# Kernel tuning notes

Hardware: AMD Instinct MI355X
Metric: run time of the kernel (lower is better)

The kernel has to match this reference:

```python
import jax, jax.numpy as jnp
import numpy as np

B, N, D = 2, 2048, 1024
H, DH = 16, 64
DI = 4096
EPS = 1e-5
NEG_SLOPE = 0.01  # F.leaky_relu default


def _ln(x, g, b):
    mu = jnp.mean(x, axis=-1, keepdims=True)
    var = jnp.mean((x - mu) ** 2, axis=-1, keepdims=True)
    return (x - mu) * jax.lax.rsqrt(var + EPS) * g + b


def setup_inputs() -> dict:
    key = jax.random.key(0)
    ks = jax.random.split(key, 10)
    s = 0.02
    return {
        "Z": jax.random.normal(ks[0], (B, N, D), jnp.float32),
        "new_mask": jax.random.normal(ks[1], (B, N, N), jnp.float32),
        "mask": jax.random.uniform(ks[2], (B, N, N), jnp.float32),
        "ln1_g": jnp.ones((D,), jnp.float32),
        "ln1_b": jnp.zeros((D,), jnp.float32),
        "qkv_w": jax.random.normal(ks[3], (3 * D, D), jnp.float32) * s,
        "qkv_b": jnp.zeros((3 * D,), jnp.float32),
        "o_w": jax.random.normal(ks[4], (D, H * DH), jnp.float32) * s,
        "ln2_g": jnp.ones((D,), jnp.float32),
        "ln2_b": jnp.zeros((D,), jnp.float32),
        "p1_w": jax.random.normal(ks[5], (DI, D), jnp.float32) * s,
        "p1_b": jnp.zeros((DI,), jnp.float32),
        "p2_w": jax.random.normal(ks[6], (D, DI), jnp.float32) * s,
        "p2_b": jnp.zeros((D,), jnp.float32),
    }


def reference(Z, new_mask, mask, ln1_g, ln1_b, qkv_w, qkv_b, o_w, ln2_g, ln2_b, p1_w, p1_b, p2_w, p2_b):
    inp = Z
    Zn = _ln(Z, ln1_g, ln1_b)
    qkv = (Zn @ qkv_w.T + qkv_b).reshape(B, N, H, 3 * DH)
    # torch chunk order in the source: V, Q, K
    V, Q, K = jnp.split(qkv, 3, axis=3)  # each [B,N,H,DH]
    # scores: einsum('bnij,bmij->binm') == [B,H,N,N]
    W = jnp.einsum("bnhd,bmhd->bhnm", Q, K) / np.sqrt(DH) + new_mask[:, None]
    A = jax.nn.softmax(W, axis=3) * mask[:, None]
    attn = jnp.einsum("bhnm,bmhd->bnhd", A, V).reshape(B, N, D)
    attn = jnp.where(attn >= 0, attn, NEG_SLOPE * attn) @ o_w.T  # leaky_relu then o_net (no bias)
    Z1 = attn + inp
    Zn2 = _ln(Z1, ln2_g, ln2_b)
    h = jax.nn.relu(Zn2 @ p1_w.T + p1_b)
    return h @ p2_w.T + p2_b + Z1
```

## Files before the change

kernel.cpp:

```cpp
#include <hip/hip_runtime.h>

typedef unsigned short u16;
typedef __attribute__((ext_vector_type(8))) short bf16x8;
typedef __attribute__((ext_vector_type(4))) float f32x4;

#define DEV static __device__ __forceinline__

DEV u16 f2bf(float f) {
    unsigned u = __float_as_uint(f);
    u += 0x7FFFu + ((u >> 16) & 1u);
    return (u16)(u >> 16);
}

typedef const __attribute__((address_space(1))) void* gas1_t;
typedef __attribute__((address_space(3))) void* gas3_t;

DEV void gl_lds16(const u16* g, u16* l) {
    __builtin_amdgcn_global_load_lds((gas1_t)g, (gas3_t)l, 16, 0, 0);
}

DEV int sw8(int row, int chunk) { return row * 64 + ((chunk ^ (row & 7)) << 3); }

__global__ void cast_bf16(const float* __restrict__ in, u16* __restrict__ out, int n4) {
    int i = blockIdx.x * blockDim.x + threadIdx.x;
    if (i < n4) {
        float4 v = ((const float4*)in)[i];
        ushort4 o;
        o.x = f2bf(v.x); o.y = f2bf(v.y); o.z = f2bf(v.z); o.w = f2bf(v.w);
        ((ushort4*)out)[i] = o;
    }
}

__global__ void cast_qkv(const float* __restrict__ in, u16* __restrict__ out) {
    int i = blockIdx.x * 256 + threadIdx.x;
    int orow = i >> 8, cc = i & 255;
    int region = orow >> 10, rem = orow & 1023, h = rem >> 6, t = rem & 63;
    int srow = h * 192 + region * 64 + t;
    float4 v = ((const float4*)in)[srow * 256 + cc];
    ushort4 o;
    o.x = f2bf(v.x); o.y = f2bf(v.y); o.z = f2bf(v.z); o.w = f2bf(v.w);
    ((ushort4*)out)[i] = o;
}

__global__ void permute_bias(const float* __restrict__ in, float* __restrict__ out) {
    int i = blockIdx.x * 256 + threadIdx.x;
    if (i < 3072) {
        int region = i >> 10, rem = i & 1023, h = rem >> 6, t = rem & 63;
        out[i] = in[h * 192 + region * 64 + t];
    }
}

__global__ void pack_mask(const float* __restrict__ nm, const float* __restrict__ pm,
                          unsigned* __restrict__ out, int n4) {
    int i = blockIdx.x * blockDim.x + threadIdx.x;
    if (i < n4) {
        float4 a = ((const float4*)nm)[i];
        float4 b = ((const float4*)pm)[i];
        uint4 o;
        o.x = ((unsigned)f2bf(b.x) << 16) | f2bf(a.x * 1.4426950f);
        o.y = ((unsigned)f2bf(b.y) << 16) | f2bf(a.y * 1.4426950f);
        o.z = ((unsigned)f2bf(b.z) << 16) | f2bf(a.z * 1.4426950f);
        o.w = ((unsigned)f2bf(b.w) << 16) | f2bf(a.w * 1.4426950f);
        ((uint4*)out)[i] = o;
    }
}

__global__ __launch_bounds__(256) void ln_bf16(const float* __restrict__ x,
                                               const float* __restrict__ gam,
                                               const float* __restrict__ bet,
                                               u16* __restrict__ y) {
    const int row = blockIdx.x;
    const int t = threadIdx.x;
    const float4 v = ((const float4*)(x + (size_t)row * 1024))[t];
    float s = v.x + v.y + v.z + v.w;
    float ss = v.x * v.x + v.y * v.y + v.z * v.z + v.w * v.w;
#pragma unroll
    for (int o = 1; o < 64; o <<= 1) {
        s += __shfl_xor(s, o);
        ss += __shfl_xor(ss, o);
    }
    __shared__ float rs[4], rss[4];
    const int wave = t >> 6, lane = t & 63;
    if (lane == 0) { rs[wave] = s; rss[wave] = ss; }
    __syncthreads();
    const float tot = rs[0] + rs[1] + rs[2] + rs[3];
    const float totss = rss[0] + rss[1] + rss[2] + rss[3];
    const float mu = tot * (1.0f / 1024.0f);
    const float var = totss * (1.0f / 1024.0f) - mu * mu;
    const float rstd = rsqrtf(var + 1e-5f);
    const float4 g4 = ((const float4*)gam)[t];
    const float4 b4 = ((const float4*)bet)[t];
    ushort4 o;
    o.x = f2bf((v.x - mu) * rstd * g4.x + b4.x);
    o.y = f2bf((v.y - mu) * rstd * g4.y + b4.y);
    o.z = f2bf((v.z - mu) * rstd * g4.z + b4.z);
    o.w = f2bf((v.w - mu) * rstd * g4.w + b4.w);
    ((ushort4*)(y + (size_t)row * 1024))[t] = o;
}

__global__ __launch_bounds__(256) void ln2_comb(const float* __restrict__ p0,
                                                const float* __restrict__ p1,
                                                const float* __restrict__ Z,
                                                const float* __restrict__ gam,
                                                const float* __restrict__ bet,
                                                float* __restrict__ Z1,
                                                u16* __restrict__ y) {
    const int row = blockIdx.x;
    const int t = threadIdx.x;
    const float4 a = ((const float4*)(p0 + (size_t)row * 1024))[t];
    const float4 c = ((const float4*)(p1 + (size_t)row * 1024))[t];
    const float4 z = ((const float4*)(Z + (size_t)row * 1024))[t];
    float4 v;
    v.x = a.x + c.x + z.x; v.y = a.y + c.y + z.y;
    v.z = a.z + c.z + z.z; v.w = a.w + c.w + z.w;
    ((float4*)(Z1 + (size_t)row * 1024))[t] = v;
    float s = v.x + v.y + v.z + v.w;
    float ss = v.x * v.x + v.y * v.y + v.z * v.z + v.w * v.w;
#pragma unroll
    for (int o = 1; o < 64; o <<= 1) {
        s += __shfl_xor(s, o);
        ss += __shfl_xor(ss, o);
    }
    __shared__ float rs[4], rss[4];
    const int wave = t >> 6, lane = t & 63;
    if (lane == 0) { rs[wave] = s; rss[wave] = ss; }
    __syncthreads();
    const float tot = rs[0] + rs[1] + rs[2] + rs[3];
    const float totss = rss[0] + rss[1] + rss[2] + rss[3];
    const float mu = tot * (1.0f / 1024.0f);
    const float var = totss * (1.0f / 1024.0f) - mu * mu;
    const float rstd = rsqrtf(var + 1e-5f);
    const float4 g4 = ((const float4*)gam)[t];
    const float4 b4 = ((const float4*)bet)[t];
    ushort4 o;
    o.x = f2bf((v.x - mu) * rstd * g4.x + b4.x);
    o.y = f2bf((v.y - mu) * rstd * g4.y + b4.y);
    o.z = f2bf((v.z - mu) * rstd * g4.z + b4.z);
    o.w = f2bf((v.w - mu) * rstd * g4.w + b4.w);
    ((ushort4*)(y + (size_t)row * 1024))[t] = o;
}

__global__ __launch_bounds__(256) void out_comb(const float* __restrict__ p0,
                                                const float* __restrict__ p1,
                                                const float* __restrict__ bias,
                                                const float* __restrict__ Z1,
                                                float* __restrict__ out) {
    int i = blockIdx.x * 256 + threadIdx.x;
    float4 a = ((const float4*)p0)[i];
    float4 c = ((const float4*)p1)[i];
    float4 z = ((const float4*)Z1)[i];
    float4 b = ((const float4*)bias)[i & 255];
    float4 o;
    o.x = a.x + c.x + z.x + b.x; o.y = a.y + c.y + z.y + b.y;
    o.z = a.z + c.z + z.z + b.z; o.w = a.w + c.w + z.w + b.w;
    ((float4*)out)[i] = o;
}

template <int EPI>
__global__ __launch_bounds__(256, 2) void gemm_bt(const u16* __restrict__ A,
                                                  const u16* __restrict__ Bt,
                                                  const float* __restrict__ bias,
                                                  void* __restrict__ out0,
                                                  void* __restrict__ out1,
                                                  void* __restrict__ out2,
                                                  int M, int N, int K, int ldk) {
    __shared__ __align__(16) u16 As[128 * 32];
    __shared__ __align__(16) u16 Bs[128 * 32];
    const int tid = threadIdx.x;
    const int wave = tid >> 6, lane = tid & 63;
    const int lhi = lane >> 4, llo = lane & 15;
    const int bx = blockIdx.x, by = blockIdx.y;
    const int kz = blockIdx.z * K;

    const int arow = wave * 32 + (lane >> 2);
    const int acol = (lane & 3) * 8;
    const u16* gA = A + (size_t)(by * 128 + arow) * ldk + kz + acol;
    const u16* gB = Bt + (size_t)(bx * 128 + arow) * ldk + kz + acol;
    u16* lA = As + wave * 1024 + lane * 8;
    u16* lB = Bs + wave * 1024 + lane * 8;

    const int wr = wave >> 1, wc = wave & 1;
    const f32x4 zero = {0.f, 0.f, 0.f, 0.f};
    f32x4 acc[4][4];
#pragma unroll
    for (int i = 0; i < 4; i++)
#pragma unroll
        for (int j = 0; j < 4; j++) acc[i][j] = zero;

    for (int k0 = 0; k0 < K; k0 += 32) {
        __syncthreads();
        gl_lds16(gA, lA);
        gl_lds16(gA + 16 * (size_t)ldk, lA + 512);
        gl_lds16(gB, lB);
        gl_lds16(gB + 16 * (size_t)ldk, lB + 512);
        gA += 32; gB += 32;
        __syncthreads();
        bf16x8 af[4], bfr[4];
#pragma unroll
        for (int i = 0; i < 4; i++)
            af[i] = *(const bf16x8*)(As + (wr * 64 + i * 16 + llo) * 32 + lhi * 8);
#pragma unroll
        for (int j = 0; j < 4; j++)
            bfr[j] = *(const bf16x8*)(Bs + (wc * 64 + j * 16 + llo) * 32 + lhi * 8);
#pragma unroll
        for (int i = 0; i < 4; i++)
#pragma unroll
            for (int j = 0; j < 4; j++)
                acc[i][j] = __builtin_amdgcn_mfma_f32_16x16x32_bf16(af[i], bfr[j], acc[i][j], 0, 0, 0);
    }

    const int rbase = by * 128 + wr * 64 + lhi * 4;
    const int cbase = bx * 128 + wc * 64 + llo;
    float* pout = (EPI == 4) ? ((float*)out0 + (size_t)blockIdx.z * M * N) : (float*)out0;
#pragma unroll
    for (int i = 0; i < 4; i++) {
#pragma unroll
        for (int j = 0; j < 4; j++) {
#pragma unroll
            for (int r = 0; r < 4; r++) {
                const int row = rbase + i * 16 + r;
                const int col = cbase + j * 16;
                float v = acc[i][j][r];
                if constexpr (EPI == 0) {
                    v += bias[col];
                    const int region = col >> 10;
                    const int c = col & 1023;
                    const int b = row >> 11, n = row & 2047;
                    if (region == 0) {
                        ((float*)out0)[(size_t)row * 1024 + c] = v;
                    } else {
                        const int h = c >> 6, t = c & 63;
                        u16* dst = (region == 1) ? (u16*)out1 : (u16*)out2;
                        dst[(((size_t)(b * 16 + h)) * 2048 + n) * 64 + t] = f2bf(v);
                    }
                } else if constexpr (EPI == 2) {
                    v += bias[col];
                    v = v > 0.f ? v : 0.f;
                    ((u16*)out0)[(size_t)row * N + col] = f2bf(v);
                } else {
                    pout[(size_t)row * N + col] = v;
                }
            }
        }
    }
}

__global__ __launch_bounds__(256) void vtrans(const float* __restrict__ Vsc,
                                              u16* __restrict__ Vt) {
    __shared__ u16 Ts[64 * 72];
    const int nt = blockIdx.x;
    const int bh = blockIdx.y;
    const int b = bh >> 4, h = bh & 15;
    const int t = threadIdx.x;
    const int n0 = nt * 64;
    const int nr = t >> 2;
    const int dq = (t & 3) * 16;
    const float* src = Vsc + ((size_t)(b * 2048 + n0 + nr)) * 1024 + h * 64 + dq;
    float4 v0 = ((const float4*)src)[0];
    float4 v1 = ((const float4*)src)[1];
    float4 v2 = ((const float4*)src)[2];
    float4 v3 = ((const float4*)src)[3];
    u16* c0 = Ts + nr;
    c0[(dq + 0) * 72]  = f2bf(v0.x); c0[(dq + 1) * 72]  = f2bf(v0.y);
    c0[(dq + 2) * 72]  = f2bf(v0.z); c0[(dq + 3) * 72]  = f2bf(v0.w);
    c0[(dq + 4) * 72]  = f2bf(v1.x); c0[(dq + 5) * 72]  = f2bf(v1.y);
    c0[(dq + 6) * 72]  = f2bf(v1.z); c0[(dq + 7) * 72]  = f2bf(v1.w);
    c0[(dq + 8) * 72]  = f2bf(v2.x); c0[(dq + 9) * 72]  = f2bf(v2.y);
    c0[(dq + 10) * 72] = f2bf(v2.z); c0[(dq + 11) * 72] = f2bf(v2.w);
    c0[(dq + 12) * 72] = f2bf(v3.x); c0[(dq + 13) * 72] = f2bf(v3.y);
    c0[(dq + 14) * 72] = f2bf(v3.z); c0[(dq + 15) * 72] = f2bf(v3.w);
    __syncthreads();
    const int d = t >> 2, n8 = (t & 3) * 16;
    bf16x8 o0 = *(const bf16x8*)(Ts + d * 72 + n8);
    bf16x8 o1 = *(const bf16x8*)(Ts + d * 72 + n8 + 8);
    u16* dst = Vt + ((size_t)bh * 64 + d) * 2048 + n0 + n8;
    *(bf16x8*)dst = o0;
    *(bf16x8*)(dst + 8) = o1;
}

__global__ __launch_bounds__(256, 4) void attn_fused4(const u16* __restrict__ Qg,
                                                      const u16* __restrict__ Kg,
                                                      const u16* __restrict__ Vt,
                                                      const unsigned* __restrict__ Mp,
                                                      u16* __restrict__ attnL) {
    __shared__ __align__(16) u16 Qs[64 * 64];
    __shared__ __align__(16) u16 Ks[64 * 64];
    __shared__ __align__(16) u16 Vs[64 * 64];
    __shared__ __align__(16) u16 Ps[64 * 72];
    const int tid = threadIdx.x, wave = tid >> 6, lane = tid & 63;
    const int lhi = lane >> 4, llo = lane & 15;
    const int id = blockIdx.x;
    const int hh = id >> 6, rem = id & 63;
    const int b = rem >> 5, qt = rem & 31;
    const int bh = b * 16 + hh;
    const int q0 = qt * 64;
    const int l3 = lane >> 3, l7 = lane & 7;
    const int swcol = (l7 ^ (l3 & 7)) * 8;

#pragma unroll
    for (int s = 0; s < 2; s++) {
        const int row = wave * 16 + s * 8 + l3;
        gl_lds16(Qg + ((size_t)bh * 2048 + q0 + row) * 64 + swcol,
                 Qs + wave * 1024 + s * 512 + lane * 8);
    }

    const unsigned* Mpb = Mp + (size_t)b * 2048 * 2048;
    int midx[4];
#pragma unroll
    for (int r = 0; r < 4; r++)
        midx[r] = (q0 + wave * 16 + lhi * 4 + r) * 2048 + llo;

    const f32x4 zero = {0.f, 0.f, 0.f, 0.f};
    f32x4 accO[4];
    float lsum[4];
#pragma unroll
    for (int j = 0; j < 4; j++) accO[j] = zero;
#pragma unroll
    for (int r = 0; r < 4; r++) lsum[r] = 0.f;

    const float CS = 0.125f * 1.4426950f;
    const int pb0 = (wave * 16 + lhi * 4) * 72 + llo;

    for (int m0 = 0; m0 < 2048; m0 += 64) {
        __syncthreads();
#pragma unroll
        for (int s = 0; s < 2; s++) {
            const int row = wave * 16 + s * 8 + l3;
            gl_lds16(Kg + ((size_t)bh * 2048 + m0 + row) * 64 + swcol,
                     Ks + wave * 1024 + s * 512 + lane * 8);
            gl_lds16(Vt + ((size_t)bh * 64 + row) * 2048 + m0 + swcol,
                     Vs + wave * 1024 + s * 512 + lane * 8);
        }
        unsigned mv[4][4];
#pragma unroll
        for (int r = 0; r < 4; r++)
#pragma unroll
            for (int j = 0; j < 4; j++) mv[r][j] = Mpb[midx[r] + m0 + j * 16];
        __syncthreads();

        f32x4 sacc[4];
#pragma unroll
        for (int j = 0; j < 4; j++) sacc[j] = zero;
#pragma unroll
        for (int kk = 0; kk < 2; kk++) {
            const bf16x8 aq = *(const bf16x8*)(Qs + sw8(wave * 16 + llo, kk * 4 + lhi));
#pragma unroll
            for (int j = 0; j < 4; j++) {
                const bf16x8 bk = *(const bf16x8*)(Ks + sw8(j * 16 + llo, kk * 4 + lhi));
                sacc[j] = __builtin_amdgcn_mfma_f32_16x16x32_bf16(aq, bk, sacc[j], 0, 0, 0);
            }
        }

#pragma unroll
        for (int j = 0; j < 4; j++)
#pragma unroll
            for (int r = 0; r < 4; r++) {
                const unsigned u = mv[r][j];
                const float nm = __uint_as_float(u << 16);
                const float pm = __uint_as_float(u & 0xFFFF0000u);
                const float e = exp2f(fmaf(sacc[j][r], CS, nm));
                lsum[r] += e;
                const float p = e * pm;
                Ps[pb0 + r * 72 + j * 16] = (u16)((__float_as_uint(p) + 0x8000u) >> 16);
            }

#pragma unroll
        for (int kk = 0; kk < 2; kk++) {
            const bf16x8 ap = *(const bf16x8*)(Ps + (wave * 16 + llo) * 72 + kk * 32 + lhi * 8);
#pragma unroll
            for (int jd = 0; jd < 4; jd++) {
                const bf16x8 bv = *(const bf16x8*)(Vs + sw8(jd * 16 + llo, kk * 4 + lhi));
                accO[jd] = __builtin_amdgcn_mfma_f32_16x16x32_bf16(ap, bv, accO[jd], 0, 0, 0);
            }
        }
    }

#pragma unroll
    for (int r = 0; r < 4; r++) {
#pragma unroll
        for (int o = 1; o < 16; o <<= 1) lsum[r] += __shfl_xor(lsum[r], o);
        lsum[r] = 1.0f / lsum[r];
    }
#pragma unroll
    for (int jd = 0; jd < 4; jd++)
#pragma unroll
        for (int r = 0; r < 4; r++) {
            float v = accO[jd][r] * lsum[r];
            v = v >= 0.f ? v : 0.01f * v;
            const int q = q0 + wave * 16 + lhi * 4 + r;
            attnL[((size_t)b * 2048 + q) * 1024 + hh * 64 + jd * 16 + llo] = f2bf(v);
        }
}

extern "C" void kernel_launch(void* const* d_in, const int* in_sizes, int n_in,
                              void* d_out, int out_size, void* d_ws, size_t ws_size,
                              hipStream_t stream) {
    const float* Z     = (const float*)d_in[0];
    const float* nmask = (const float*)d_in[1];
    const float* pmask = (const float*)d_in[2];
    const float* ln1_g = (const float*)d_in[3];
    const float* ln1_b = (const float*)d_in[4];
    const float* qkv_w = (const float*)d_in[5];
    const float* qkv_b = (const float*)d_in[6];
    const float* o_w   = (const float*)d_in[7];
    const float* ln2_g = (const float*)d_in[8];
    const float* ln2_b = (const float*)d_in[9];
    const float* p1_w  = (const float*)d_in[10];
    const float* p1_b  = (const float*)d_in[11];
    const float* p2_w  = (const float*)d_in[12];
    const float* p2_b  = (const float*)d_in[13];
    float* out = (float*)d_out;

    char* w = (char*)d_ws;
    auto take = [&](size_t bytes) -> char* {
        char* p = w;
        w += (bytes + 255) & ~(size_t)255;
        return p;
    };
    u16* qkvW   = (u16*)take((size_t)3072 * 1024 * 2);
    u16* oW     = (u16*)take((size_t)1024 * 1024 * 2);
    u16* p1W    = (u16*)take((size_t)4096 * 1024 * 2);
    u16* p2W    = (u16*)take((size_t)1024 * 4096 * 2);
    u16* Zn     = (u16*)take((size_t)4096 * 1024 * 2);
    u16* Qb     = (u16*)take((size_t)32 * 2048 * 64 * 2);
    u16* Kb     = (u16*)take((size_t)32 * 2048 * 64 * 2);
    u16* Vt     = (u16*)take((size_t)32 * 64 * 2048 * 2);
    u16* attnL  = (u16*)take((size_t)4096 * 1024 * 2);
    float* Z1   = (float*)take((size_t)4096 * 1024 * 4);
    u16* hbuf   = (u16*)take((size_t)4096 * 4096 * 2);
    unsigned* Mp = (unsigned*)take((size_t)2 * 2048 * 2048 * 4);
    float* pbias = (float*)take((size_t)3072 * 4);
    float* Vsc   = (float*)hbuf;
    float* part  = (float*)Mp;
    float* part1 = part + (size_t)4096 * 1024;

    cast_qkv<<<dim3(3072), 256, 0, stream>>>(qkv_w, qkvW);
    permute_bias<<<dim3(12), 256, 0, stream>>>(qkv_b, pbias);
    cast_bf16<<<dim3(1024), 256, 0, stream>>>(o_w, oW, 1024 * 1024 / 4);
    cast_bf16<<<dim3(4096), 256, 0, stream>>>(p1_w, p1W, 4096 * 1024 / 4);
    cast_bf16<<<dim3(4096), 256, 0, stream>>>(p2_w, p2W, 1024 * 4096 / 4);
    pack_mask<<<dim3(8192), 256, 0, stream>>>(nmask, pmask, Mp, 2 * 2048 * 2048 / 4);

    ln_bf16<<<dim3(4096), 256, 0, stream>>>(Z, ln1_g, ln1_b, Zn);
    gemm_bt<0><<<dim3(24, 32), 256, 0, stream>>>(Zn, qkvW, pbias, Vsc, Qb, Kb, 4096, 3072, 1024, 1024);
    vtrans<<<dim3(32, 32), 256, 0, stream>>>(Vsc, Vt);
    attn_fused4<<<dim3(1024), 256, 0, stream>>>(Qb, Kb, Vt, Mp, attnL);
    gemm_bt<4><<<dim3(8, 32, 2), 256, 0, stream>>>(attnL, oW, nullptr, part, nullptr, nullptr, 4096, 1024, 512, 1024);
    ln2_comb<<<dim3(4096), 256, 0, stream>>>(part, part1, Z, ln2_g, ln2_b, Z1, Zn);
    gemm_bt<2><<<dim3(32, 32), 256, 0, stream>>>(Zn, p1W, p1_b, hbuf, nullptr, nullptr, 4096, 4096, 1024, 1024);
    gemm_bt<4><<<dim3(8, 32, 2), 256, 0, stream>>>(hbuf, p2W, nullptr, part, nullptr, nullptr, 4096, 1024, 2048, 4096);
    out_comb<<<dim3(4096), 256, 0, stream>>>(part, part1, p2_b, Z1, out);
}
```

Baseline: 445.5 us.

## Merge prep kernels, split o-proj GEMM four ways, raise GEMM occupancy

Folds the six weight/mask preparation kernels into one launch dispatched by block range. The output-projection GEMM gets a 4-way K split, writing partials into two buffers, and the LN2 combine now sums four partials. GEMM launch bounds move from 2 to 3 blocks per CU, and the attention probability conversion to bf16 drops rounding in favour of truncation. These target launch overhead and under-filled GPU waves in the small GEMM. They trade extra partial-buffer traffic, possible register spills, and slightly lower precision.

```diff
diff --git a/kernel.cpp b/kernel.cpp
--- a/kernel.cpp
+++ b/kernel.cpp
@@ -21,39 +21,49 @@
 
 DEV int sw8(int row, int chunk) { return row * 64 + ((chunk ^ (row & 7)) << 3); }
 
-__global__ void cast_bf16(const float* __restrict__ in, u16* __restrict__ out, int n4) {
-    int i = blockIdx.x * blockDim.x + threadIdx.x;
-    if (i < n4) {
-        float4 v = ((const float4*)in)[i];
+__global__ __launch_bounds__(256) void prep_all(const float* __restrict__ qkv_w,
+                                                const float* __restrict__ o_w,
+                                                const float* __restrict__ p1_w,
+                                                const float* __restrict__ p2_w,
+                                                const float* __restrict__ qkv_b,
+                                                const float* __restrict__ nm,
+                                                const float* __restrict__ pm,
+                                                u16* __restrict__ qkvW,
+                                                u16* __restrict__ oW,
+                                                u16* __restrict__ p1W,
+                                                u16* __restrict__ p2W,
+                                                float* __restrict__ pbias,
+                                                unsigned* __restrict__ Mp) {
+    const int bid = blockIdx.x, t = threadIdx.x;
+    if (bid < 3072) {
+        int i = bid * 256 + t;
+        int orow = i >> 8, cc = i & 255;
+        int region = orow >> 10, rem = orow & 1023, h = rem >> 6, tt = rem & 63;
+        int srow = h * 192 + region * 64 + tt;
+        float4 v = ((const float4*)qkv_w)[srow * 256 + cc];
         ushort4 o;
         o.x = f2bf(v.x); o.y = f2bf(v.y); o.z = f2bf(v.z); o.w = f2bf(v.w);
-        ((ushort4*)out)[i] = o;
-    }
-}
-
-__global__ void cast_qkv(const float* __restrict__ in, u16* __restrict__ out) {
-    int i = blockIdx.x * 256 + threadIdx.x;
-    int orow = i >> 8, cc = i & 255;
-    int region = orow >> 10, rem = orow & 1023, h = rem >> 6, t = rem & 63;
-    int srow = h * 192 + region * 64 + t;
-    float4 v = ((const float4*)in)[srow * 256 + cc];
-    ushort4 o;
-    o.x = f2bf(v.x); o.y = f2bf(v.y); o.z = f2bf(v.z); o.w = f2bf(v.w);
-    ((ushort4*)out)[i] = o;
-}
-
-__global__ void permute_bias(const float* __restrict__ in, float* __restrict__ out) {
-    int i = blockIdx.x * 256 + threadIdx.x;
-    if (i < 3072) {
-        int region = i >> 10, rem = i & 1023, h = rem >> 6, t = rem & 63;
-        out[i] = in[h * 192 + region * 64 + t];
-    }
-}
-
-__global__ void pack_mask(const float* __restrict__ nm, const float* __restrict__ pm,
-                          unsigned* __restrict__ out, int n4) {
-    int i = blockIdx.x * blockDim.x + threadIdx.x;
-    if (i < n4) {
+        ((ushort4*)qkvW)[i] = o;
+    } else if (bid < 4096) {
+        int i = (bid - 3072) * 256 + t;
+        float4 v = ((const float4*)o_w)[i];
+        ushort4 o;
+        o.x = f2bf(v.x); o.y = f2bf(v.y); o.z = f2bf(v.z); o.w = f2bf(v.w);
+        ((ushort4*)oW)[i] = o;
+    } else if (bid < 8192) {
+        int i = (bid - 4096) * 256 + t;
+        float4 v = ((const float4*)p1_w)[i];
+        ushort4 o;
+        o.x = f2bf(v.x); o.y = f2bf(v.y); o.z = f2bf(v.z); o.w = f2bf(v.w);
+        ((ushort4*)p1W)[i] = o;
+    } else if (bid < 12288) {
+        int i = (bid - 8192) * 256 + t;
+        float4 v = ((const float4*)p2_w)[i];
+        ushort4 o;
+        o.x = f2bf(v.x); o.y = f2bf(v.y); o.z = f2bf(v.z); o.w = f2bf(v.w);
+        ((ushort4*)p2W)[i] = o;
+    } else if (bid < 20480) {
+        int i = (bid - 12288) * 256 + t;
         float4 a = ((const float4*)nm)[i];
         float4 b = ((const float4*)pm)[i];
         uint4 o;
@@ -61,7 +71,14 @@
         o.y = ((unsigned)f2bf(b.y) << 16) | f2bf(a.y * 1.4426950f);
         o.z = ((unsigned)f2bf(b.z) << 16) | f2bf(a.z * 1.4426950f);
         o.w = ((unsigned)f2bf(b.w) << 16) | f2bf(a.w * 1.4426950f);
-        ((uint4*)out)[i] = o;
+        ((uint4*)Mp)[i] = o;
+    } else {
+#pragma unroll
+        for (int k = 0; k < 12; k++) {
+            int i = k * 256 + t;
+            int region = i >> 10, rem = i & 1023, h = rem >> 6, tt = rem & 63;
+            pbias[i] = qkv_b[h * 192 + region * 64 + tt];
+        }
     }
 }
 
@@ -98,22 +115,29 @@
     ((ushort4*)(y + (size_t)row * 1024))[t] = o;
 }
 
-__global__ __launch_bounds__(256) void ln2_comb(const float* __restrict__ p0,
-                                                const float* __restrict__ p1,
-                                                const float* __restrict__ Z,
-                                                const float* __restrict__ gam,
-                                                const float* __restrict__ bet,
-                                                float* __restrict__ Z1,
-                                                u16* __restrict__ y) {
+__global__ __launch_bounds__(256) void ln2_comb4(const float* __restrict__ p0,
+                                                 const float* __restrict__ p1,
+                                                 const float* __restrict__ p2,
+                                                 const float* __restrict__ p3,
+                                                 const float* __restrict__ Z,
+                                                 const float* __restrict__ gam,
+                                                 const float* __restrict__ bet,
+                                                 float* __restrict__ Z1,
+                                                 u16* __restrict__ y) {
     const int row = blockIdx.x;
     const int t = threadIdx.x;
-    const float4 a = ((const float4*)(p0 + (size_t)row * 1024))[t];
-    const float4 c = ((const float4*)(p1 + (size_t)row * 1024))[t];
-    const float4 z = ((const float4*)(Z + (size_t)row * 1024))[t];
+    const size_t off = (size_t)row * 256 + t;
+    const float4 a = ((const float4*)p0)[off];
+    const float4 c = ((const float4*)p1)[off];
+    const float4 d = ((const float4*)p2)[off];
+    const float4 e = ((const float4*)p3)[off];
+    const float4 z = ((const float4*)Z)[off];
     float4 v;
-    v.x = a.x + c.x + z.x; v.y = a.y + c.y + z.y;
-    v.z = a.z + c.z + z.z; v.w = a.w + c.w + z.w;
-    ((float4*)(Z1 + (size_t)row * 1024))[t] = v;
+    v.x = a.x + c.x + d.x + e.x + z.x;
+    v.y = a.y + c.y + d.y + e.y + z.y;
+    v.z = a.z + c.z + d.z + e.z + z.z;
+    v.w = a.w + c.w + d.w + e.w + z.w;
+    ((float4*)Z1)[off] = v;
     float s = v.x + v.y + v.z + v.w;
     float ss = v.x * v.x + v.y * v.y + v.z * v.z + v.w * v.w;
 #pragma unroll
@@ -157,7 +181,7 @@
 }
 
 template <int EPI>
-__global__ __launch_bounds__(256, 2) void gemm_bt(const u16* __restrict__ A,
+__global__ __launch_bounds__(256, 3) void gemm_bt(const u16* __restrict__ A,
                                                   const u16* __restrict__ Bt,
                                                   const float* __restrict__ bias,
                                                   void* __restrict__ out0,
@@ -211,7 +235,11 @@
 
     const int rbase = by * 128 + wr * 64 + lhi * 4;
     const int cbase = bx * 128 + wc * 64 + llo;
-    float* pout = (EPI == 4) ? ((float*)out0 + (size_t)blockIdx.z * M * N) : (float*)out0;
+    float* pout = nullptr;
+    if constexpr (EPI == 4) {
+        pout = (blockIdx.z < 2) ? ((float*)out0 + (size_t)blockIdx.z * M * N)
+                                : ((float*)out1 + (size_t)(blockIdx.z - 2) * M * N);
+    }
 #pragma unroll
     for (int i = 0; i < 4; i++) {
 #pragma unroll
@@ -361,7 +389,7 @@
                 const float e = exp2f(fmaf(sacc[j][r], CS, nm));
                 lsum[r] += e;
                 const float p = e * pm;
-                Ps[pb0 + r * 72 + j * 16] = (u16)((__float_as_uint(p) + 0x8000u) >> 16);
+                Ps[pb0 + r * 72 + j * 16] = (u16)(__float_as_uint(p) >> 16);
             }
 
 #pragma unroll
@@ -430,24 +458,24 @@
     u16* hbuf   = (u16*)take((size_t)4096 * 4096 * 2);
     unsigned* Mp = (unsigned*)take((size_t)2 * 2048 * 2048 * 4);
     float* pbias = (float*)take((size_t)3072 * 4);
-    float* Vsc   = (float*)hbuf;
-    float* part  = (float*)Mp;
-    float* part1 = part + (size_t)4096 * 1024;
-
-    cast_qkv<<<dim3(3072), 256, 0, stream>>>(qkv_w, qkvW);
-    permute_bias<<<dim3(12), 256, 0, stream>>>(qkv_b, pbias);
-    cast_bf16<<<dim3(1024), 256, 0, stream>>>(o_w, oW, 1024 * 1024 / 4);
-    cast_bf16<<<dim3(4096), 256, 0, stream>>>(p1_w, p1W, 4096 * 1024 / 4);
-    cast_bf16<<<dim3(4096), 256, 0, stream>>>(p2_w, p2W, 1024 * 4096 / 4);
-    pack_mask<<<dim3(8192), 256, 0, stream>>>(nmask, pmask, Mp, 2 * 2048 * 2048 / 4);
-
+    float* Vsc    = (float*)hbuf;
+    float* part01 = (float*)Mp;
+    float* part23 = (float*)hbuf;
+
+    prep_all<<<dim3(20481), 256, 0, stream>>>(qkv_w, o_w, p1_w, p2_w, qkv_b, nmask, pmask,
+                                              qkvW, oW, p1W, p2W, pbias, Mp);
     ln_bf16<<<dim3(4096), 256, 0, stream>>>(Z, ln1_g, ln1_b, Zn);
     gemm_bt<0><<<dim3(24, 32), 256, 0, stream>>>(Zn, qkvW, pbias, Vsc, Qb, Kb, 4096, 3072, 1024, 1024);
     vtrans<<<dim3(32, 32), 256, 0, stream>>>(Vsc, Vt);
     attn_fused4<<<dim3(1024), 256, 0, stream>>>(Qb, Kb, Vt, Mp, attnL);
-    gemm_bt<4><<<dim3(8, 32, 2), 256, 0, stream>>>(attnL, oW, nullptr, part, nullptr, nullptr, 4096, 1024, 512, 1024);
-    ln2_comb<<<dim3(4096), 256, 0, stream>>>(part, part1, Z, ln2_g, ln2_b, Z1, Zn);
-    gemm_bt<2><<<dim3(32, 32), 256, 0, stream>>>(Zn, p1W, p1_b, hbuf, nullptr, nullptr, 4096, 4096, 1024, 1024);
-    gemm_bt<4><<<dim3(8, 32, 2), 256, 0, stream>>>(hbuf, p2W, nullptr, part, nullptr, nullptr, 4096, 1024, 2048, 4096);
-    out_comb<<<dim3(4096), 256, 0, stream>>>(part, part1, p2_b, Z1, out);
-}
+    gemm_bt<4><<<dim3(8, 32, 4), 256, 0, stream>>>(attnL, oW, nullptr, part01, part23, nullptr,
+                                                   4096, 1024, 256, 1024);
+    ln2_comb4<<<dim3(4096), 256, 0, stream>>>(part01, part01 + (size_t)4096 * 1024,
+                                              part23, part23 + (size_t)4096 * 1024,
+                                              Z, ln2_g, ln2_b, Z1, Zn);
+    gemm_bt<2><<<dim3(32, 32), 256, 0, stream>>>(Zn, p1W, p1_b, hbuf, nullptr, nullptr,
+                                                 4096, 4096, 1024, 1024);
+    gemm_bt<4><<<dim3(8, 32, 2), 256, 0, stream>>>(hbuf, p2W, nullptr, part01, nullptr, nullptr,
+                                                   4096, 1024, 2048, 4096);
+    out_comb<<<dim3(4096), 256, 0, stream>>>(part01, part01 + (size_t)4096 * 1024, p2_b, Z1, out);
+}
```

Result: no change. 443.8 us (-0.4%).
